# Optimization experiments

Hardware: AMD Instinct MI355X
Metric: run time of the kernel (lower is better)

## Reference

```python
import jax, jax.numpy as jnp
import numpy as np

NEG_SLOPE = 0.01  # torch LeakyReLU default
MIN_FREQ = 1.0
MAX_FREQ = 10.0
W = 100
N_HIDDEN = 100
N_OBS = 64

def _leaky(x):
    return jnp.where(x >= 0, x, NEG_SLOPE * x)

def setup_inputs() -> dict:
    key = jax.random.key(0)
    ks = jax.random.split(key, 7)
    # kaiming_uniform-ish init scales (exact init doesn't matter for correctness baseline)
    def unif(k, shape, fan_in):
        bound = np.sqrt(6.0 / fan_in)
        return jax.random.uniform(k, shape, jnp.float32, -bound, bound)
    x = jax.random.normal(ks[0], (65536, N_OBS), jnp.float32)
    W_in = unif(ks[1], (N_OBS, W), N_OBS)
    b_in = jnp.zeros((W,), jnp.float32)
    Ws = unif(ks[2], (N_HIDDEN, W, W), W)
    bs = jnp.zeros((N_HIDDEN, W), jnp.float32)
    W_out = unif(ks[3], (W, 1), W)
    b_out = jnp.zeros((1,), jnp.float32)
    return {"x": x, "W_in": W_in, "b_in": b_in, "Ws": Ws, "bs": bs,
            "W_out": W_out, "b_out": b_out}

def reference(x, W_in, b_in, Ws, bs, W_out, b_out):
    h = _leaky(x @ W_in + b_in)                       # [B, 100]
    def layer(h, wb):
        w, b = wb
        return _leaky(h @ w + b), None
    h, _ = jax.lax.scan(layer, h, (Ws, bs))           # 100 hidden layers
    a = h @ W_out + b_out                             # [B, 1]
    a = jnp.tanh(a)
    return (a + 1.0) / 2.0 * (MAX_FREQ - MIN_FREQ) + MIN_FREQ
```

## Files before the change

kernel.cpp:

```cpp
#include <hip/hip_runtime.h>
#include <cmath>

#define NLAYERS 100
#define DIN     64
#define WDIM    100
#define NTT     4
#define NTW     2
#define ROWS    32
#define KS      7
#define PSTR    136
#define BUF     (ROWS * PSTR)

typedef _Float16 half8  __attribute__((ext_vector_type(8)));
typedef _Float16 half2v __attribute__((ext_vector_type(2)));
typedef __fp16   fp16x2 __attribute__((ext_vector_type(2)));
typedef float    f32x4  __attribute__((ext_vector_type(4)));
typedef float    f32x16 __attribute__((ext_vector_type(16)));

#define WSH_LAYER_HALVES (KS * NTT * 64 * 8)
#define WSH_HALVES       (NLAYERS * WSH_LAYER_HALVES)
#define W0_HALVES        (4 * NTT * 64 * 8)
#define BPAD_FLOATS      128
#define OFF_BPAD_B       ((WSH_HALVES + W0_HALVES) * 2)
#define OFF_WOUT_B       (OFF_BPAD_B + BPAD_FLOATS * 4)
#define WOUT_FLOATS      128

__global__ __launch_bounds__(256)
void actor_prep(const float* __restrict__ Win, const float* __restrict__ bin,
                const float* __restrict__ Ws,  const float* __restrict__ bs,
                const float* __restrict__ Wout,
                _Float16* __restrict__ wsh, _Float16* __restrict__ w0sh,
                float* __restrict__ bpad, float* __restrict__ woutp) {
    __shared__ float tile[16 * 128];
    const int bid = blockIdx.x, tid = threadIdx.x;
    if (bid < NLAYERS * KS) {
        const int l = bid / KS, ks = bid % KS;
#pragma unroll
        for (int e = 0; e < 8; ++e) {
            int idx = tid + 256 * e;
            int kk = idx >> 7, nn = idx & 127;
            int k = ks * 16 + kk;
            float v = 0.f;
            if (k < WDIM && nn < WDIM)        v = Ws[(l * WDIM + k) * WDIM + nn];
            else if (k == WDIM && nn < WDIM)  v = bs[l * WDIM + nn];
            else if (k == WDIM && nn == WDIM) v = 1.0f;
            tile[idx] = v;
        }
        __syncthreads();
        const int lane = tid & 63, nt = tid >> 6;
        const int g = lane >> 5, n = nt * 32 + (lane & 31);
        half8 o;
#pragma unroll
        for (int j = 0; j < 8; ++j) o[j] = (_Float16)tile[(g * 8 + j) * 128 + n];
        *(half8*)(wsh + (((l * KS + ks) * NTT + nt) << 9) + lane * 8) = o;
        return;
    }
    int b2 = bid - NLAYERS * KS;
    if (b2 < 4) {
        const int ks = b2;
#pragma unroll
        for (int e = 0; e < 8; ++e) {
            int idx = tid + 256 * e;
            int kk = idx >> 7, nn = idx & 127;
            int k = ks * 16 + kk;
            tile[idx] = (nn < WDIM) ? Win[k * WDIM + nn] : 0.f;
        }
        __syncthreads();
        const int lane = tid & 63, nt = tid >> 6;
        const int g = lane >> 5, n = nt * 32 + (lane & 31);
        half8 o;
#pragma unroll
        for (int j = 0; j < 8; ++j) o[j] = (_Float16)tile[(g * 8 + j) * 128 + n];
        *(half8*)(w0sh + ((ks * NTT + nt) << 9) + lane * 8) = o;
        return;
    }
    if (tid < BPAD_FLOATS) {
        bpad[tid] = (tid < WDIM) ? bin[tid] : (tid == WDIM ? 1.0f : 0.f);
    } else {
        int t = tid - BPAD_FLOATS;
        if (t < WOUT_FLOATS) woutp[t] = (t < WDIM) ? Wout[t] : 0.f;
    }
}

__device__ __forceinline__ void split8(const float* __restrict__ p, half8& hi, half8& lo) {
    f32x4 u0 = *(const f32x4*)p;
    f32x4 u1 = *(const f32x4*)(p + 4);
    float v[8] = {u0[0], u0[1], u0[2], u0[3], u1[0], u1[1], u1[2], u1[3]};
#pragma unroll
    for (int e = 0; e < 8; e += 2) {
        fp16x2 h = __builtin_amdgcn_cvt_pkrtz(v[e], v[e + 1]);
        float r0 = v[e]     - (float)h[0];
        float r1 = v[e + 1] - (float)h[1];
        fp16x2 l = __builtin_amdgcn_cvt_pkrtz(r0, r1);
        hi[e] = (_Float16)h[0]; hi[e + 1] = (_Float16)h[1];
        lo[e] = (_Float16)l[0]; lo[e + 1] = (_Float16)l[1];
    }
}

__device__ __forceinline__ void ep_quad(const f32x16 a, int qd, _Float16* __restrict__ d) {
    half2v p01, p23;
    p01[0] = (_Float16)a[4 * qd + 0]; p01[1] = (_Float16)a[4 * qd + 1];
    p23[0] = (_Float16)a[4 * qd + 2]; p23[1] = (_Float16)a[4 * qd + 3];
    const half2v slope = {(_Float16)0.01f, (_Float16)0.01f};
    p01 = __builtin_elementwise_max(p01, p01 * slope);
    p23 = __builtin_elementwise_max(p23, p23 * slope);
    uint2 w;
    w.x = __builtin_bit_cast(unsigned, p01);
    w.y = __builtin_bit_cast(unsigned, p23);
    *reinterpret_cast<uint2*>(d) = w;
}

__global__ __launch_bounds__(128, 4)
void actor_main(const float* __restrict__ x,
                const _Float16* __restrict__ wsh,
                const _Float16* __restrict__ w0sh,
                const float* __restrict__ bpad,
                const float* __restrict__ woutp,
                const float* __restrict__ bout,
                float* __restrict__ out) {
    __shared__ __align__(16) _Float16 hp[2 * BUF];
    const int lane = threadIdx.x & 63;
    const int wid  = threadIdx.x >> 6;
    const int g = lane >> 5, b31 = lane & 31;
    const int sw = ((b31 >> 3) & 1) << 5;
    const int rowbase = blockIdx.x * ROWS;
    const int ntb = wid * NTW;

    f32x16 acc[NTW];
    half8 wb[KS][NTW];
    const f32x16 zero16 = {0,0,0,0, 0,0,0,0, 0,0,0,0, 0,0,0,0};

    {
        half8 w0[4][NTW];
#pragma unroll
        for (int ks = 0; ks < 4; ++ks)
#pragma unroll
            for (int ntl = 0; ntl < NTW; ++ntl)
                w0[ks][ntl] = *(const half8*)(w0sh + (ks * NTT + ntb + ntl) * 512 + lane * 8);
#pragma unroll
        for (int ntl = 0; ntl < NTW; ++ntl)
#pragma unroll
            for (int qd = 0; qd < 4; ++qd) {
                f32x4 tq = *(const f32x4*)(bpad + (ntb + ntl) * 32 + 8 * qd + 4 * g);
#pragma unroll
                for (int r = 0; r < 4; ++r) acc[ntl][4 * qd + r] = tq[r];
            }
        const float* xr = x + (rowbase + b31) * DIN;
#pragma unroll
        for (int ks = 0; ks < 4; ++ks) {
            half8 xhi, xlo;
            split8(xr + ks * 16 + g * 8, xhi, xlo);
#pragma unroll
            for (int ntl = 0; ntl < NTW; ++ntl) {
                acc[ntl] = __builtin_amdgcn_mfma_f32_32x32x16_f16(w0[ks][ntl], xhi, acc[ntl], 0, 0, 0);
                acc[ntl] = __builtin_amdgcn_mfma_f32_32x32x16_f16(w0[ks][ntl], xlo, acc[ntl], 0, 0, 0);
            }
        }
    }
#pragma unroll
    for (int ntl = 0; ntl < NTW; ++ntl) {
        _Float16* d = hp + b31 * PSTR + (((ntb + ntl) * 32 + 4 * g) ^ sw);
#pragma unroll
        for (int qd = 0; qd < 4; ++qd) ep_quad(acc[ntl], qd, d + 8 * qd);
    }
#pragma unroll
    for (int ks = 0; ks < KS; ++ks)
#pragma unroll
        for (int ntl = 0; ntl < NTW; ++ntl)
            wb[ks][ntl] = *(const half8*)(wsh + (ks * NTT + ntb + ntl) * 512 + lane * 8);
    asm volatile("s_waitcnt lgkmcnt(0)\n\ts_barrier" ::: "memory");

#pragma unroll 1
    for (int l = 0; l < NLAYERS; ++l) {
        const _Float16* rb = hp + (l & 1) * BUF;
        _Float16* wbf = hp + ((l + 1) & 1) * BUF;
        const _Float16* wn = wsh + (l < NLAYERS - 1 ? l + 1 : l) * WSH_LAYER_HALVES;
        half8 bh[KS];

#pragma unroll
        for (int ks = 0; ks < KS; ++ks)
            bh[ks] = *(const half8*)(rb + b31 * PSTR + ((ks * 16 + g * 8) ^ sw));
#pragma unroll
        for (int ks = 0; ks < KS; ++ks) {
            acc[0] = __builtin_amdgcn_mfma_f32_32x32x16_f16(
                wb[ks][0], bh[ks], (ks == 0 ? zero16 : acc[0]), 0, 0, 0);
            acc[1] = __builtin_amdgcn_mfma_f32_32x32x16_f16(
                wb[ks][1], bh[ks], (ks == 0 ? zero16 : acc[1]), 0, 0, 0);
            wb[ks][0] = *(const half8*)(wn + (ks * NTT + ntb + 0) * 512 + lane * 8);
            wb[ks][1] = *(const half8*)(wn + (ks * NTT + ntb + 1) * 512 + lane * 8);
        }
        {
            _Float16* d0 = wbf + b31 * PSTR + (((ntb + 0) * 32 + 4 * g) ^ sw);
            _Float16* d1 = wbf + b31 * PSTR + (((ntb + 1) * 32 + 4 * g) ^ sw);
#pragma unroll
            for (int qd = 0; qd < 4; ++qd) {
                ep_quad(acc[0], qd, d0 + 8 * qd);
                ep_quad(acc[1], qd, d1 + 8 * qd);
            }
        }
        asm volatile("s_waitcnt lgkmcnt(0)\n\ts_barrier" ::: "memory");
    }

    float s = 0.f;
#pragma unroll
    for (int ntl = 0; ntl < NTW; ++ntl)
#pragma unroll
        for (int qd = 0; qd < 4; ++qd) {
            f32x4 w4 = *(const f32x4*)(woutp + (ntb + ntl) * 32 + 8 * qd + 4 * g);
#pragma unroll
            for (int r = 0; r < 4; ++r) {
                float a = acc[ntl][4 * qd + r];
                float v = fmaxf(a, 0.01f * a);
                s += v * w4[r];
            }
        }
    s += __shfl_xor(s, 32);
    float* red = (float*)hp;
    if (lane < 32) red[wid * 32 + b31] = s;
    __syncthreads();
    if (threadIdx.x < 32) {
        const int r = threadIdx.x;
        float tot = red[r] + red[32 + r] + bout[0];
        out[rowbase + r] = tanhf(tot) * 4.5f + 5.5f;
    }
}

extern "C" void kernel_launch(void* const* d_in, const int* in_sizes, int n_in,
                              void* d_out, int out_size, void* d_ws, size_t ws_size,
                              hipStream_t stream) {
    const float* x    = (const float*)d_in[0];
    const float* Win  = (const float*)d_in[1];
    const float* bin  = (const float*)d_in[2];
    const float* Ws   = (const float*)d_in[3];
    const float* bs   = (const float*)d_in[4];
    const float* Wout = (const float*)d_in[5];
    const float* bout = (const float*)d_in[6];
    float* out = (float*)d_out;

    char* ws = (char*)d_ws;
    _Float16* wsh  = (_Float16*)ws;
    _Float16* w0sh = wsh + WSH_HALVES;
    float* bpad  = (float*)(ws + OFF_BPAD_B);
    float* woutp = (float*)(ws + OFF_WOUT_B);

    hipLaunchKernelGGL(actor_prep, dim3(NLAYERS * KS + 4 + 1), dim3(256), 0, stream,
                       Win, bin, Ws, bs, Wout, wsh, w0sh, bpad, woutp);

    const int nrows = in_sizes[0] / DIN;
    hipLaunchKernelGGL(actor_main, dim3(nrows / ROWS), dim3(128), 0, stream,
                       x, wsh, w0sh, bpad, woutp, bout, out);
}
```

Before: 302.8 us.

## Use one wave per 32-row tile computing all four column tiles without barriers

Changes the work split so a single 64-lane wave owns a whole 32-row block and computes all four N tiles per layer. This removes the per-layer block barrier, the double-buffered activation LDS, the XOR swizzle, and the cross-wave output reduction. In exchange each wave holds twice as many weight and accumulator registers, occupancy drops, and LDS bank conflicts may return without the swizzle. Within one wave, ordering of the LDS write-then-read across layers relies on in-order LDS behaviour.

```diff
diff --git a/kernel.cpp b/kernel.cpp
--- a/kernel.cpp
+++ b/kernel.cpp
@@ -5,7 +5,6 @@
 #define DIN     64
 #define WDIM    100
 #define NTT     4
-#define NTW     2
 #define ROWS    32
 #define KS      7
 #define PSTR    136
@@ -110,7 +109,7 @@
     *reinterpret_cast<uint2*>(d) = w;
 }
 
-__global__ __launch_bounds__(128, 4)
+__global__ __launch_bounds__(64, 2)
 void actor_main(const float* __restrict__ x,
                 const _Float16* __restrict__ wsh,
                 const _Float16* __restrict__ w0sh,
@@ -118,32 +117,29 @@
                 const float* __restrict__ woutp,
                 const float* __restrict__ bout,
                 float* __restrict__ out) {
-    __shared__ __align__(16) _Float16 hp[2 * BUF];
-    const int lane = threadIdx.x & 63;
-    const int wid  = threadIdx.x >> 6;
+    __shared__ __align__(16) _Float16 hp[BUF];
+    const int lane = threadIdx.x;
     const int g = lane >> 5, b31 = lane & 31;
-    const int sw = ((b31 >> 3) & 1) << 5;
     const int rowbase = blockIdx.x * ROWS;
-    const int ntb = wid * NTW;
-
-    f32x16 acc[NTW];
-    half8 wb[KS][NTW];
+
+    f32x16 acc[NTT];
+    half8 wb[KS][NTT];
     const f32x16 zero16 = {0,0,0,0, 0,0,0,0, 0,0,0,0, 0,0,0,0};
 
     {
-        half8 w0[4][NTW];
+        half8 w0[4][NTT];
 #pragma unroll
         for (int ks = 0; ks < 4; ++ks)
 #pragma unroll
-            for (int ntl = 0; ntl < NTW; ++ntl)
-                w0[ks][ntl] = *(const half8*)(w0sh + (ks * NTT + ntb + ntl) * 512 + lane * 8);
-#pragma unroll
-        for (int ntl = 0; ntl < NTW; ++ntl)
+            for (int nt = 0; nt < NTT; ++nt)
+                w0[ks][nt] = *(const half8*)(w0sh + (ks * NTT + nt) * 512 + lane * 8);
+#pragma unroll
+        for (int nt = 0; nt < NTT; ++nt)
 #pragma unroll
             for (int qd = 0; qd < 4; ++qd) {
-                f32x4 tq = *(const f32x4*)(bpad + (ntb + ntl) * 32 + 8 * qd + 4 * g);
-#pragma unroll
-                for (int r = 0; r < 4; ++r) acc[ntl][4 * qd + r] = tq[r];
+                f32x4 tq = *(const f32x4*)(bpad + nt * 32 + 8 * qd + 4 * g);
+#pragma unroll
+                for (int r = 0; r < 4; ++r) acc[nt][4 * qd + r] = tq[r];
             }
         const float* xr = x + (rowbase + b31) * DIN;
 #pragma unroll
@@ -151,77 +147,70 @@
             half8 xhi, xlo;
             split8(xr + ks * 16 + g * 8, xhi, xlo);
 #pragma unroll
-            for (int ntl = 0; ntl < NTW; ++ntl) {
-                acc[ntl] = __builtin_amdgcn_mfma_f32_32x32x16_f16(w0[ks][ntl], xhi, acc[ntl], 0, 0, 0);
-                acc[ntl] = __builtin_amdgcn_mfma_f32_32x32x16_f16(w0[ks][ntl], xlo, acc[ntl], 0, 0, 0);
+            for (int nt = 0; nt < NTT; ++nt) {
+                acc[nt] = __builtin_amdgcn_mfma_f32_32x32x16_f16(w0[ks][nt], xhi, acc[nt], 0, 0, 0);
+                acc[nt] = __builtin_amdgcn_mfma_f32_32x32x16_f16(w0[ks][nt], xlo, acc[nt], 0, 0, 0);
             }
         }
     }
 #pragma unroll
-    for (int ntl = 0; ntl < NTW; ++ntl) {
-        _Float16* d = hp + b31 * PSTR + (((ntb + ntl) * 32 + 4 * g) ^ sw);
-#pragma unroll
-        for (int qd = 0; qd < 4; ++qd) ep_quad(acc[ntl], qd, d + 8 * qd);
+    for (int nt = 0; nt < NTT; ++nt) {
+        _Float16* d = hp + b31 * PSTR + nt * 32 + 4 * g;
+#pragma unroll
+        for (int qd = 0; qd < 4; ++qd) ep_quad(acc[nt], qd, d + 8 * qd);
     }
 #pragma unroll
     for (int ks = 0; ks < KS; ++ks)
 #pragma unroll
-        for (int ntl = 0; ntl < NTW; ++ntl)
-            wb[ks][ntl] = *(const half8*)(wsh + (ks * NTT + ntb + ntl) * 512 + lane * 8);
-    asm volatile("s_waitcnt lgkmcnt(0)\n\ts_barrier" ::: "memory");
+        for (int nt = 0; nt < NTT; ++nt)
+            wb[ks][nt] = *(const half8*)(wsh + (ks * NTT + nt) * 512 + lane * 8);
 
 #pragma unroll 1
     for (int l = 0; l < NLAYERS; ++l) {
-        const _Float16* rb = hp + (l & 1) * BUF;
-        _Float16* wbf = hp + ((l + 1) & 1) * BUF;
         const _Float16* wn = wsh + (l < NLAYERS - 1 ? l + 1 : l) * WSH_LAYER_HALVES;
         half8 bh[KS];
-
 #pragma unroll
         for (int ks = 0; ks < KS; ++ks)
-            bh[ks] = *(const half8*)(rb + b31 * PSTR + ((ks * 16 + g * 8) ^ sw));
+            bh[ks] = *(const half8*)(hp + b31 * PSTR + ks * 16 + g * 8);
 #pragma unroll
         for (int ks = 0; ks < KS; ++ks) {
             acc[0] = __builtin_amdgcn_mfma_f32_32x32x16_f16(
                 wb[ks][0], bh[ks], (ks == 0 ? zero16 : acc[0]), 0, 0, 0);
             acc[1] = __builtin_amdgcn_mfma_f32_32x32x16_f16(
                 wb[ks][1], bh[ks], (ks == 0 ? zero16 : acc[1]), 0, 0, 0);
-            wb[ks][0] = *(const half8*)(wn + (ks * NTT + ntb + 0) * 512 + lane * 8);
-            wb[ks][1] = *(const half8*)(wn + (ks * NTT + ntb + 1) * 512 + lane * 8);
-        }
-        {
-            _Float16* d0 = wbf + b31 * PSTR + (((ntb + 0) * 32 + 4 * g) ^ sw);
-            _Float16* d1 = wbf + b31 * PSTR + (((ntb + 1) * 32 + 4 * g) ^ sw);
-#pragma unroll
-            for (int qd = 0; qd < 4; ++qd) {
-                ep_quad(acc[0], qd, d0 + 8 * qd);
-                ep_quad(acc[1], qd, d1 + 8 * qd);
-            }
-        }
-        asm volatile("s_waitcnt lgkmcnt(0)\n\ts_barrier" ::: "memory");
+            acc[2] = __builtin_amdgcn_mfma_f32_32x32x16_f16(
+                wb[ks][2], bh[ks], (ks == 0 ? zero16 : acc[2]), 0, 0, 0);
+            acc[3] = __builtin_amdgcn_mfma_f32_32x32x16_f16(
+                wb[ks][3], bh[ks], (ks == 0 ? zero16 : acc[3]), 0, 0, 0);
+#pragma unroll
+            for (int nt = 0; nt < NTT; ++nt)
+                wb[ks][nt] = *(const half8*)(wn + (ks * NTT + nt) * 512 + lane * 8);
+        }
+#pragma unroll
+        for (int nt = 0; nt < NTT; ++nt) {
+            _Float16* d = hp + b31 * PSTR + nt * 32 + 4 * g;
+#pragma unroll
+            for (int qd = 0; qd < 4; ++qd) ep_quad(acc[nt], qd, d + 8 * qd);
+        }
     }
 
     float s = 0.f;
 #pragma unroll
-    for (int ntl = 0; ntl < NTW; ++ntl)
+    for (int nt = 0; nt < NTT; ++nt)
 #pragma unroll
         for (int qd = 0; qd < 4; ++qd) {
-            f32x4 w4 = *(const f32x4*)(woutp + (ntb + ntl) * 32 + 8 * qd + 4 * g);
+            f32x4 w4 = *(const f32x4*)(woutp + nt * 32 + 8 * qd + 4 * g);
 #pragma unroll
             for (int r = 0; r < 4; ++r) {
-                float a = acc[ntl][4 * qd + r];
+                float a = acc[nt][4 * qd + r];
                 float v = fmaxf(a, 0.01f * a);
                 s += v * w4[r];
             }
         }
     s += __shfl_xor(s, 32);
-    float* red = (float*)hp;
-    if (lane < 32) red[wid * 32 + b31] = s;
-    __syncthreads();
-    if (threadIdx.x < 32) {
-        const int r = threadIdx.x;
-        float tot = red[r] + red[32 + r] + bout[0];
-        out[rowbase + r] = tanhf(tot) * 4.5f + 5.5f;
+    if (lane < 32) {
+        float tot = s + bout[0];
+        out[rowbase + b31] = tanhf(tot) * 4.5f + 5.5f;
     }
 }
 
@@ -247,6 +236,6 @@
                        Win, bin, Ws, bs, Wout, wsh, w0sh, bpad, woutp);
 
     const int nrows = in_sizes[0] / DIN;
-    hipLaunchKernelGGL(actor_main, dim3(nrows / ROWS), dim3(128), 0, stream,
+    hipLaunchKernelGGL(actor_main, dim3(nrows / ROWS), dim3(64), 0, stream,
                        x, wsh, w0sh, bpad, woutp, bout, out);
 }
```

New measurement: 299.7 us. Within noise of the previous version (-1.0%).
